# Kernel optimization log

Measured on AMD Instinct MI355X. Metric: run time of the kernel, lower is better.

The kernel has to match this reference:

```python
import jax, jax.numpy as jnp
import numpy as np
from jax import lax

J2 = -1.0
J4 = 0.5
KT = 0.5
DT = 0.01
SIGMA = float(np.sqrt(2.0 * KT * DT))  # noise scale per Euler-Maruyama step


def setup_inputs() -> dict:
    key = jax.random.key(0)
    k_x, = jax.random.split(key, 1)
    n_samples, n_dim = 2048, 256
    x0 = jax.random.normal(k_x, (n_samples, n_dim), dtype=jnp.float32)
    b = jnp.zeros((n_dim,), dtype=jnp.float32)  # learned bias parameter
    return {"x0": x0, "b": b, "n_steps": 500}


def reference(x0, b, n_steps):
    # Langevin dynamics: x <- x - grad_V(x)*dt + sqrt(2 kT dt)*N(0,1)
    # grad_V(x) = 2*J2*x + 4*J4*x^3 + b
    keys = jax.random.split(jax.random.key(1), n_steps)

    def step(x, k):
        grad = 2.0 * J2 * x + 4.0 * J4 * x * x * x + b
        noise = jax.random.normal(k, x.shape, x.dtype) * SIGMA
        return x - grad * DT + noise, None

    x, _ = lax.scan(step, x0, keys)
    return x
```

## Files before the change

### kernel.cpp

```cpp
#include <hip/hip_runtime.h>


#define TF_ROUND(x0, x1, R)                                   \
  {                                                           \
    x0 += x1;                                                 \
    x1 = ((x1 << (R)) | (x1 >> (32 - (R))));                  \
    x1 ^= x0;                                                 \
  }

__device__ __forceinline__ void tf2x32(unsigned k0, unsigned k1,
                                       unsigned c0, unsigned c1,
                                       unsigned& o0, unsigned& o1) {
  const unsigned k2 = k0 ^ k1 ^ 0x1BD11BDAu;
  unsigned x0 = c0 + k0;
  unsigned x1 = c1 + k1;
  TF_ROUND(x0, x1, 13) TF_ROUND(x0, x1, 15) TF_ROUND(x0, x1, 26) TF_ROUND(x0, x1, 6)
  x0 += k1; x1 += k2 + 1u;
  TF_ROUND(x0, x1, 17) TF_ROUND(x0, x1, 29) TF_ROUND(x0, x1, 16) TF_ROUND(x0, x1, 24)
  x0 += k2; x1 += k0 + 2u;
  TF_ROUND(x0, x1, 13) TF_ROUND(x0, x1, 15) TF_ROUND(x0, x1, 26) TF_ROUND(x0, x1, 6)
  x0 += k0; x1 += k1 + 3u;
  TF_ROUND(x0, x1, 17) TF_ROUND(x0, x1, 29) TF_ROUND(x0, x1, 16) TF_ROUND(x0, x1, 24)
  x0 += k1; x1 += k2 + 4u;
  TF_ROUND(x0, x1, 13) TF_ROUND(x0, x1, 15) TF_ROUND(x0, x1, 26) TF_ROUND(x0, x1, 6)
  x0 += k2; x1 += k0 + 5u;
  o0 = x0;
  o1 = x1;
}

__device__ __forceinline__ float bits_to_normal(unsigned bits) {
  const float f = __uint_as_float((bits >> 9) | 0x3F800000u) - 1.0f;
  const float lo = -0.99999994f;
  const float u = fmaf(f, 2.0f, lo);
  const float m = u * u;
  const float t = 1.0f - m;
  const float l = __log2f(t);
  float w = fmaf(l, -0.69314718246459961f, l * 1.9046543e-09f);
  float p;
  if (w < 5.0f) {
    w = w - 2.5f;
    p = 2.81022636e-08f;
    p = fmaf(p, w, 3.43273939e-07f);
    p = fmaf(p, w, -3.5233877e-06f);
    p = fmaf(p, w, -4.39150654e-06f);
    p = fmaf(p, w, 0.00021858087f);
    p = fmaf(p, w, -0.00125372503f);
    p = fmaf(p, w, -0.00417768164f);
    p = fmaf(p, w, 0.246640727f);
    p = fmaf(p, w, 1.50140941f);
  } else {
    w = sqrtf(w) - 3.0f;
    p = -0.000200214257f;
    p = fmaf(p, w, 0.000100950558f);
    p = fmaf(p, w, 0.00134934322f);
    p = fmaf(p, w, -0.00367342844f);
    p = fmaf(p, w, 0.00573950773f);
    p = fmaf(p, w, -0.0076224613f);
    p = fmaf(p, w, 0.00943887047f);
    p = fmaf(p, w, 1.00167406f);
    p = fmaf(p, w, 2.83297682f);
  }
  return __uint_as_float(0x3FB504F3u) * (p * u);
}

__global__ __launch_bounds__(256, 8) void langevin_tf(
    const float* __restrict__ x0, const float* __restrict__ bias,
    const int* __restrict__ nsteps_p, float* __restrict__ out,
    int N, int ndim) {
  __shared__ uint2 skeys[1025];
  const int n_steps = __builtin_amdgcn_readfirstlane(nsteps_p[0]);
  const int nfill = n_steps < 1024 ? n_steps : 1024;
  for (int l = (int)threadIdx.x; l < nfill; l += (int)blockDim.x) {
    unsigned o0, o1;
    tf2x32(0u, 1u, 0u, (unsigned)l, o0, o1);
    skeys[l] = make_uint2(o0, o1);
  }
  __syncthreads();

  const int j = (int)(blockIdx.x * blockDim.x + threadIdx.x);
  if (j >= N) return;
  const unsigned cj = (unsigned)j;
  float x = x0[j];
  const float b = bias[j % ndim];

  uint2 kc = skeys[0];
#pragma unroll 2
  for (int t = 0; t < n_steps; ++t) {
    const uint2 kn = skeys[t + 1];
    unsigned r0, r1;
    tf2x32(kc.x, kc.y, 0u, cj, r0, r1);
    const float nz = bits_to_normal(r0 ^ r1);
    const float g = -2.0f * x + ((2.0f * x) * x) * x + b;
    x = (x - g * 0.01f) + nz * 0.1f;
    kc = kn;
  }
  out[j] = x;
}

extern "C" void kernel_launch(void* const* d_in, const int* in_sizes, int n_in,
                              void* d_out, int out_size, void* d_ws, size_t ws_size,
                              hipStream_t stream) {
  (void)n_in; (void)d_ws; (void)ws_size; (void)out_size;
  const float* x0 = (const float*)d_in[0];
  const float* b = (const float*)d_in[1];
  const int* ns = (const int*)d_in[2];
  float* out = (float*)d_out;

  const int n = in_sizes[0];
  const int ndim = in_sizes[1];
  const int block = 256;
  const int grid = (n + block - 1) / block;
  hipLaunchKernelGGL(langevin_tf, dim3(grid), dim3(block), 0, stream,
                     x0, b, ns, out, n, ndim);
}
```

Measured before the change: 607.9 us.

## Precompute per-step Threefry key schedule in LDS and make normal transform branchless

```diff
diff --git a/kernel.cpp b/kernel.cpp
--- a/kernel.cpp
+++ b/kernel.cpp
@@ -1,98 +1,122 @@
 #include <hip/hip_runtime.h>
 
 
-#define TF_ROUND(x0, x1, R)                                   \
-  {                                                           \
-    x0 += x1;                                                 \
-    x1 = ((x1 << (R)) | (x1 >> (32 - (R))));                  \
-    x1 ^= x0;                                                 \
-  }
+__device__ __forceinline__ void tf_r4a(unsigned& x0, unsigned& x1) {
+  x0 += x1; x1 = (x1 << 13) | (x1 >> 19); x1 ^= x0;
+  x0 += x1; x1 = (x1 << 15) | (x1 >> 17); x1 ^= x0;
+  x0 += x1; x1 = (x1 << 26) | (x1 >> 6);  x1 ^= x0;
+  x0 += x1; x1 = (x1 << 6)  | (x1 >> 26); x1 ^= x0;
+}
+__device__ __forceinline__ void tf_r4b(unsigned& x0, unsigned& x1) {
+  x0 += x1; x1 = (x1 << 17) | (x1 >> 15); x1 ^= x0;
+  x0 += x1; x1 = (x1 << 29) | (x1 >> 3);  x1 ^= x0;
+  x0 += x1; x1 = (x1 << 16) | (x1 >> 16); x1 ^= x0;
+  x0 += x1; x1 = (x1 << 24) | (x1 >> 8);  x1 ^= x0;
+}
 
 __device__ __forceinline__ void tf2x32(unsigned k0, unsigned k1,
                                        unsigned c0, unsigned c1,
                                        unsigned& o0, unsigned& o1) {
   const unsigned k2 = k0 ^ k1 ^ 0x1BD11BDAu;
-  unsigned x0 = c0 + k0;
-  unsigned x1 = c1 + k1;
-  TF_ROUND(x0, x1, 13) TF_ROUND(x0, x1, 15) TF_ROUND(x0, x1, 26) TF_ROUND(x0, x1, 6)
-  x0 += k1; x1 += k2 + 1u;
-  TF_ROUND(x0, x1, 17) TF_ROUND(x0, x1, 29) TF_ROUND(x0, x1, 16) TF_ROUND(x0, x1, 24)
-  x0 += k2; x1 += k0 + 2u;
-  TF_ROUND(x0, x1, 13) TF_ROUND(x0, x1, 15) TF_ROUND(x0, x1, 26) TF_ROUND(x0, x1, 6)
-  x0 += k0; x1 += k1 + 3u;
-  TF_ROUND(x0, x1, 17) TF_ROUND(x0, x1, 29) TF_ROUND(x0, x1, 16) TF_ROUND(x0, x1, 24)
-  x0 += k1; x1 += k2 + 4u;
-  TF_ROUND(x0, x1, 13) TF_ROUND(x0, x1, 15) TF_ROUND(x0, x1, 26) TF_ROUND(x0, x1, 6)
-  x0 += k2; x1 += k0 + 5u;
-  o0 = x0;
-  o1 = x1;
+  unsigned x0 = c0 + k0, x1 = c1 + k1;
+  tf_r4a(x0, x1); x0 += k1; x1 += k2 + 1u;
+  tf_r4b(x0, x1); x0 += k2; x1 += k0 + 2u;
+  tf_r4a(x0, x1); x0 += k0; x1 += k1 + 3u;
+  tf_r4b(x0, x1); x0 += k1; x1 += k2 + 4u;
+  tf_r4a(x0, x1); x0 += k2; x1 += k0 + 5u;
+  o0 = x0; o1 = x1;
+}
+
+__device__ __forceinline__ unsigned tf_fold(const unsigned w[8], unsigned c1) {
+  unsigned x0 = w[0], x1 = c1 + w[1];
+  tf_r4a(x0, x1); x0 += w[1]; x1 += w[3];
+  tf_r4b(x0, x1); x0 += w[2]; x1 += w[4];
+  tf_r4a(x0, x1); x0 += w[0]; x1 += w[5];
+  tf_r4b(x0, x1); x0 += w[1]; x1 += w[6];
+  tf_r4a(x0, x1); x0 += w[2]; x1 += w[7];
+  return x0 ^ x1;
 }
 
 __device__ __forceinline__ float bits_to_normal(unsigned bits) {
   const float f = __uint_as_float((bits >> 9) | 0x3F800000u) - 1.0f;
-  const float lo = -0.99999994f;
-  const float u = fmaf(f, 2.0f, lo);
+  const float u = fmaf(f, 2.0f, -0.99999994f);
   const float m = u * u;
-  const float t = 1.0f - m;
-  const float l = __log2f(t);
-  float w = fmaf(l, -0.69314718246459961f, l * 1.9046543e-09f);
-  float p;
-  if (w < 5.0f) {
-    w = w - 2.5f;
-    p = 2.81022636e-08f;
-    p = fmaf(p, w, 3.43273939e-07f);
-    p = fmaf(p, w, -3.5233877e-06f);
-    p = fmaf(p, w, -4.39150654e-06f);
-    p = fmaf(p, w, 0.00021858087f);
-    p = fmaf(p, w, -0.00125372503f);
-    p = fmaf(p, w, -0.00417768164f);
-    p = fmaf(p, w, 0.246640727f);
-    p = fmaf(p, w, 1.50140941f);
-  } else {
-    w = sqrtf(w) - 3.0f;
-    p = -0.000200214257f;
-    p = fmaf(p, w, 0.000100950558f);
-    p = fmaf(p, w, 0.00134934322f);
-    p = fmaf(p, w, -0.00367342844f);
-    p = fmaf(p, w, 0.00573950773f);
-    p = fmaf(p, w, -0.0076224613f);
-    p = fmaf(p, w, 0.00943887047f);
-    p = fmaf(p, w, 1.00167406f);
-    p = fmaf(p, w, 2.83297682f);
-  }
+  const float l = __log2f(1.0f - m);
+  const float w = fmaf(l, -0.69314718246459961f, l * 1.9046543e-09f);
+  const bool s = w < 5.0f;
+  const float za = w - 2.5f;
+  const float zb = __builtin_amdgcn_sqrtf(w) - 3.0f;
+  const float z = s ? za : zb;
+  float p =          s ? 2.81022636e-08f  : -0.000200214257f;
+  p = fmaf(p, z,     s ? 3.43273939e-07f  :  0.000100950558f);
+  p = fmaf(p, z,     s ? -3.5233877e-06f  :  0.00134934322f);
+  p = fmaf(p, z,     s ? -4.39150654e-06f : -0.00367342844f);
+  p = fmaf(p, z,     s ? 0.00021858087f   :  0.00573950773f);
+  p = fmaf(p, z,     s ? -0.00125372503f  : -0.0076224613f);
+  p = fmaf(p, z,     s ? -0.00417768164f  :  0.00943887047f);
+  p = fmaf(p, z,     s ? 0.246640727f     :  1.00167406f);
+  p = fmaf(p, z,     s ? 1.50140941f      :  2.83297682f);
   return __uint_as_float(0x3FB504F3u) * (p * u);
 }
 
 __global__ __launch_bounds__(256, 8) void langevin_tf(
-    const float* __restrict__ x0, const float* __restrict__ bias,
+    const float* __restrict__ x0p, const float* __restrict__ bias,
     const int* __restrict__ nsteps_p, float* __restrict__ out,
     int N, int ndim) {
-  __shared__ uint2 skeys[1025];
+  __shared__ __align__(16) unsigned skeys[512 * 8];
   const int n_steps = __builtin_amdgcn_readfirstlane(nsteps_p[0]);
-  const int nfill = n_steps < 1024 ? n_steps : 1024;
+  const int nfill = n_steps < 512 ? n_steps : 512;
   for (int l = (int)threadIdx.x; l < nfill; l += (int)blockDim.x) {
     unsigned o0, o1;
     tf2x32(0u, 1u, 0u, (unsigned)l, o0, o1);
-    skeys[l] = make_uint2(o0, o1);
+    const unsigned k2 = o0 ^ o1 ^ 0x1BD11BDAu;
+    unsigned* wp = &skeys[8 * l];
+    wp[0] = o0;       wp[1] = o1;       wp[2] = k2;       wp[3] = k2 + 1u;
+    wp[4] = o0 + 2u;  wp[5] = o1 + 3u;  wp[6] = k2 + 4u;  wp[7] = o0 + 5u;
   }
   __syncthreads();
 
   const int j = (int)(blockIdx.x * blockDim.x + threadIdx.x);
   if (j >= N) return;
   const unsigned cj = (unsigned)j;
-  float x = x0[j];
+  float x = x0p[j];
   const float b = bias[j % ndim];
 
-  uint2 kc = skeys[0];
-#pragma unroll 2
-  for (int t = 0; t < n_steps; ++t) {
-    const uint2 kn = skeys[t + 1];
-    unsigned r0, r1;
-    tf2x32(kc.x, kc.y, 0u, cj, r0, r1);
-    const float nz = bits_to_normal(r0 ^ r1);
-    const float g = -2.0f * x + ((2.0f * x) * x) * x + b;
-    x = (x - g * 0.01f) + nz * 0.1f;
-    kc = kn;
+  if (n_steps <= 512) {
+    int t = 0;
+#pragma unroll 1
+    for (; t + 1 < n_steps; t += 2) {
+      unsigned wa[8], wb[8];
+      *(uint4*)&wa[0] = *(const uint4*)&skeys[8 * t];
+      *(uint4*)&wa[4] = *(const uint4*)&skeys[8 * t + 4];
+      *(uint4*)&wb[0] = *(const uint4*)&skeys[8 * t + 8];
+      *(uint4*)&wb[4] = *(const uint4*)&skeys[8 * t + 12];
+      const unsigned ra = tf_fold(wa, cj);
+      const unsigned rb = tf_fold(wb, cj);
+      const float na = bits_to_normal(ra);
+      const float nb = bits_to_normal(rb);
+      float g = -2.0f * x + ((2.0f * x) * x) * x + b;
+      x = (x - g * 0.01f) + na * 0.1f;
+      g = -2.0f * x + ((2.0f * x) * x) * x + b;
+      x = (x - g * 0.01f) + nb * 0.1f;
+    }
+    if (t < n_steps) {
+      unsigned wa[8];
+      *(uint4*)&wa[0] = *(const uint4*)&skeys[8 * t];
+      *(uint4*)&wa[4] = *(const uint4*)&skeys[8 * t + 4];
+      const float na = bits_to_normal(tf_fold(wa, cj));
+      const float g = -2.0f * x + ((2.0f * x) * x) * x + b;
+      x = (x - g * 0.01f) + na * 0.1f;
+    }
+  } else {
+    for (int t = 0; t < n_steps; ++t) {
+      unsigned o0, o1, r0, r1;
+      tf2x32(0u, 1u, 0u, (unsigned)t, o0, o1);
+      tf2x32(o0, o1, 0u, cj, r0, r1);
+      const float nz = bits_to_normal(r0 ^ r1);
+      const float g = -2.0f * x + ((2.0f * x) * x) * x + b;
+      x = (x - g * 0.01f) + nz * 0.1f;
+    }
   }
   out[j] = x;
 }
```

After: 601.9 us. No clear change (-1.0%).
